# Kernel tuning notes

Hardware: AMD Instinct MI355X
Metric: run time of the kernel (lower is better)

## Reference

```python
import jax, jax.numpy as jnp
import numpy as np

TAU = 0.07
K = 50
EPS = 1e-8


def _flat_norm(x):
    # [B, C, H, W] -> [B*H*W, C], L2-normalized along C
    B, C = x.shape[0], x.shape[1]
    x = jnp.moveaxis(x, 1, -1).reshape(-1, C)
    n = jnp.linalg.norm(x, axis=-1, keepdims=True)
    return x / jnp.maximum(n, 1e-12)


def setup_inputs() -> dict:
    key = jax.random.key(0)
    ks = jax.random.split(key, 5)
    shp = (2, 128, 64, 64)
    lshp = (2, 4, 64, 64)
    return {
        "input": jax.random.normal(ks[0], shp, dtype=jnp.float32),
        "positive": jax.random.normal(ks[1], shp, dtype=jnp.float32),
        "negative": jax.random.normal(ks[2], shp, dtype=jnp.float32),
        "input_logits": jax.random.normal(ks[3], lshp, dtype=jnp.float32),
        "negative_logits": jax.random.normal(ks[4], lshp, dtype=jnp.float32),
    }


def reference(input, positive, negative, input_logits, negative_logits):
    norm_input = _flat_norm(input)        # [N, C]
    norm_positive = _flat_norm(positive)  # [N, C]
    norm_negative = _flat_norm(negative)  # [N, C]

    # check_input: multi-class logits branch (softmax over class dim, then max)
    in_probs = jax.nn.softmax(input_logits, axis=1)
    neg_probs = jax.nn.softmax(negative_logits, axis=1)
    seg_input = jnp.argmax(in_probs, axis=1).reshape(-1)       # [N] int
    seg_negative = jnp.argmax(neg_probs, axis=1).reshape(-1)   # [N] int
    negative_prob = jnp.max(neg_probs, axis=1).reshape(-1)     # [N] float

    # positive cosine similarity (unit vectors -> dot product)
    pos_sim = jnp.sum(norm_input * norm_positive, axis=-1)     # [N]

    # mask[i, j] = (seg_input[j] != seg_negative[i]) * negative_prob[i]
    diff = (seg_input[None, :] != seg_negative[:, None]).astype(jnp.float16)
    masked = diff.astype(jnp.float32) * negative_prob[:, None]  # [N, N]

    # top-k over dim=0 (negatives) for each input column j -> indices [N, K]
    _, idx = jax.lax.top_k(masked.T, K)                         # [N, K]
    sampled = norm_negative[idx]                                # [N, K, C]

    neg_sim = jnp.einsum('nkc,nc->nk', sampled, norm_input)     # [N, K]
    nominator = jnp.exp(pos_sim / TAU)                          # [N]
    denominator = jnp.sum(jnp.exp(neg_sim / TAU), axis=1) + nominator
    loss = -jnp.mean(jnp.log(nominator / (denominator + EPS)))

    alter_sim = jnp.einsum('nkc,nc->nk', sampled, norm_positive)
    alter_den = jnp.sum(jnp.exp(alter_sim / TAU), axis=1) + nominator
    alter_loss = -jnp.mean(jnp.log(nominator / (alter_den + EPS)))

    return loss + alter_loss
```

## Files before the change

### kernel.cpp

```cpp
#include <hip/hip_runtime.h>
#include <math.h>

#define TAU_INV (1.0f / 0.07f)
#define KSEL 50
#define KPAD 64
#define NPIX 8192
#define CCH 128
#define HWSZ 4096
#define NCLS 4
#define EPSL 1e-8f
#define NBINS 1026
#define PXT 32
#define SROW 132

__global__ void __launch_bounds__(256) mega_kernel(
        const float* __restrict__ input, const float* __restrict__ positive,
        const float* __restrict__ negative,
        const float* __restrict__ ilog, const float* __restrict__ nlog,
        float* __restrict__ ni, float* __restrict__ np_, float* __restrict__ nn,
        int* __restrict__ seg_in, int* __restrict__ seg_neg,
        float* __restrict__ neg_prob) {
    __shared__ float tile[CCH][65];
    __shared__ float partial[4][64];
    __shared__ float invn[64];

    int t = threadIdx.x;
    int blk = blockIdx.x;

    if (blk < 384) {
        int tensor = blk >> 7, chunk = blk & 127;
        const float* src = (tensor == 0) ? input : (tensor == 1) ? positive : negative;
        float*       dst = (tensor == 0) ? ni    : (tensor == 1) ? np_      : nn;

        int n0 = chunk * 64;
        int b = n0 >> 12, hw0 = n0 & (HWSZ - 1);
        const float* base = src + (size_t)b * CCH * HWSZ + hw0;

        #pragma unroll
        for (int i = 0; i < 8; ++i) {
            int lin = t + i * 256;
            int c = lin >> 4, hwq = (lin & 15) * 4;
            float4 v = *(const float4*)&base[(size_t)c * HWSZ + hwq];
            tile[c][hwq + 0] = v.x; tile[c][hwq + 1] = v.y;
            tile[c][hwq + 2] = v.z; tile[c][hwq + 3] = v.w;
        }
        __syncthreads();

        int nof = t & 63, part = t >> 6;
        float s = 0.f;
        #pragma unroll
        for (int j = 0; j < 32; ++j) {
            float v = tile[part * 32 + j][nof];
            s += v * v;
        }
        partial[part][nof] = s;
        __syncthreads();
        if (t < 64) {
            float tot = partial[0][t] + partial[1][t] + partial[2][t] + partial[3][t];
            invn[t] = 1.0f / fmaxf(sqrtf(tot), 1e-12f);
        }
        __syncthreads();

        #pragma unroll
        for (int i = 0; i < 8; ++i) {
            int lin = t + i * 256;
            int nf = lin >> 5, cq = (lin & 31) * 4;
            float inv = invn[nf];
            float4 o;
            o.x = tile[cq + 0][nf] * inv;
            o.y = tile[cq + 1][nf] * inv;
            o.z = tile[cq + 2][nf] * inv;
            o.w = tile[cq + 3][nf] * inv;
            *(float4*)&dst[(size_t)(n0 + nf) * CCH + cq] = o;
        }
    } else {
        int n0 = ((blk - 384) * 256 + t) * 4;
        int b = n0 >> 12, hw = n0 & (HWSZ - 1);

        const float* pi = ilog + (size_t)b * NCLS * HWSZ + hw;
        float4 a0 = *(const float4*)&pi[0];
        float4 a1 = *(const float4*)&pi[HWSZ];
        float4 a2 = *(const float4*)&pi[2 * HWSZ];
        float4 a3 = *(const float4*)&pi[3 * HWSZ];
        const float* pn = nlog + (size_t)b * NCLS * HWSZ + hw;
        float4 b0 = *(const float4*)&pn[0];
        float4 b1 = *(const float4*)&pn[HWSZ];
        float4 b2 = *(const float4*)&pn[2 * HWSZ];
        float4 b3 = *(const float4*)&pn[3 * HWSZ];

        int4 si4, sn4; float4 npb;
        const float* A0 = (const float*)&a0; const float* A1 = (const float*)&a1;
        const float* A2 = (const float*)&a2; const float* A3 = (const float*)&a3;
        const float* B0 = (const float*)&b0; const float* B1 = (const float*)&b1;
        const float* B2 = (const float*)&b2; const float* B3 = (const float*)&b3;
        int* SI = (int*)&si4; int* SN = (int*)&sn4; float* NP = (float*)&npb;
        #pragma unroll
        for (int j = 0; j < 4; ++j) {
            float l0 = A0[j], l1 = A1[j], l2 = A2[j], l3 = A3[j];
            int bi = 0; float bv = l0;
            if (l1 > bv) { bv = l1; bi = 1; }
            if (l2 > bv) { bv = l2; bi = 2; }
            if (l3 > bv) { bv = l3; bi = 3; }
            SI[j] = bi;
            float m0 = B0[j], m1 = B1[j], m2 = B2[j], m3 = B3[j];
            int ci = 0; float cv = m0;
            if (m1 > cv) { cv = m1; ci = 1; }
            if (m2 > cv) { cv = m2; ci = 2; }
            if (m3 > cv) { cv = m3; ci = 3; }
            SN[j] = ci;
            float s = expf(m0 - cv) + expf(m1 - cv) + expf(m2 - cv) + expf(m3 - cv);
            NP[j] = 1.0f / s;
        }
        *(int4*)&seg_in[n0] = si4;
        *(int4*)&seg_neg[n0] = sn4;
        *(float4*)&neg_prob[n0] = npb;
    }
}

__global__ void __launch_bounds__(1024) topk_kernel(
        const int* __restrict__ seg_in, const int* __restrict__ seg_neg,
        const float* __restrict__ neg_prob,
        int* __restrict__ topk, int* __restrict__ perm, int* __restrict__ cnt,
        float* __restrict__ out) {
    __shared__ unsigned hist[NBINS];
    __shared__ unsigned coarse[33];
    __shared__ unsigned long long cand[2048];
    __shared__ unsigned above_cnt, cand_cnt, bucket_cnt;
    __shared__ int sB, sc0;

    int c = blockIdx.x, t = threadIdx.x;
    if (c == 0 && t == 0) out[0] = 0.0f;

    for (int i = t; i < NBINS; i += 1024) hist[i] = 0;
    if (t < 33) coarse[t] = 0;
    if (t == 0) { above_cnt = 0; cand_cnt = 0; bucket_cnt = 0; }
    __syncthreads();

    unsigned keys[8]; int bins[8];
    #pragma unroll
    for (int s = 0; s < 2; ++s) {
        int i4 = (t + s * 1024) * 4;
        int4 sn = *(const int4*)&seg_neg[i4];
        int4 sg = *(const int4*)&seg_in[i4];
        float4 npv = *(const float4*)&neg_prob[i4];
        const int* SN = (const int*)&sn;
        const int* SG = (const int*)&sg;
        const float* NP = (const float*)&npv;
        #pragma unroll
        for (int j = 0; j < 4; ++j) {
            float v = (SN[j] != c) ? NP[j] : 0.0f;
            unsigned key = __float_as_uint(v);
            int bin = (key < 0x3E800000u) ? 0 : (int)(1u + ((key - 0x3E800000u) >> 14));
            keys[s * 4 + j] = key; bins[s * 4 + j] = bin;
            atomicAdd(&hist[bin], 1u);
            if (SG[j] == c) {
                unsigned p = atomicAdd(&bucket_cnt, 1u);
                perm[c * NPIX + p] = i4 + j;
            }
        }
    }
    __syncthreads();
    if (t == 0) cnt[c] = (int)bucket_cnt;

    for (int i = t; i < NBINS; i += 1024) atomicAdd(&coarse[i >> 5], hist[i]);
    __syncthreads();

    if (t == 0) {
        unsigned cum = 0; int j = 32;
        for (; j > 0; --j) {
            unsigned h = coarse[j];
            if (cum + h >= KSEL) break;
            cum += h;
        }
        int hi = j * 32 + 31; if (hi > NBINS - 1) hi = NBINS - 1;
        int B = 0;
        for (int b = hi; b >= j * 32; --b) {
            unsigned h = hist[b];
            if (cum + h >= KSEL) { B = b; break; }
            cum += h;
        }
        sB = B; sc0 = (int)cum;
    }
    __syncthreads();
    int B = sB, c0 = sc0;

    #pragma unroll
    for (int s = 0; s < 8; ++s) {
        int i = (t + (s >> 2) * 1024) * 4 + (s & 3);
        if (bins[s] > B) {
            unsigned pos = atomicAdd(&above_cnt, 1u);
            topk[c * KSEL + pos] = i;
        } else if (bins[s] == B) {
            unsigned j = atomicAdd(&cand_cnt, 1u);
            if (j < 2048)
                cand[j] = ((unsigned long long)keys[s] << 32) |
                          (unsigned long long)(0xFFFFFFFFu - (unsigned)i);
        }
    }
    __syncthreads();

    int m = KSEL - c0;
    int cb = (int)cand_cnt; if (cb > 2048) cb = 2048;
    if (t < 64) {
        for (int r = 0; r < m; ++r) {
            unsigned long long best = 0;
            for (int j = t; j < cb; j += 64) {
                unsigned long long v = cand[j];
                if (v > best) best = v;
            }
            #pragma unroll
            for (int off = 32; off; off >>= 1) {
                unsigned long long o = __shfl_xor(best, off);
                if (o > best) best = o;
            }
            if (t == 0) topk[c * KSEL + c0 + r] = (int)(0xFFFFFFFFu - (unsigned)(best & 0xFFFFFFFFull));
            for (int j = t; j < cb; j += 64)
                if (cand[j] == best) cand[j] = 0;
        }
    }
}

__global__ void __launch_bounds__(256) loss_kernel(
        const float* __restrict__ ni, const float* __restrict__ npos,
        const float* __restrict__ nn, const int* __restrict__ topk,
        const int* __restrict__ perm, const int* __restrict__ cnt,
        float* __restrict__ out) {
    __shared__ float Sl[KPAD * SROW];
    __shared__ float Xl[PXT * SROW];
    __shared__ float Pl[PXT * SROW];
    __shared__ float bsum[4];

    int c = blockIdx.y;
    int count = cnt[c];
    int start = blockIdx.x * PXT;
    if (start >= count) return;
    int t = threadIdx.x;

    {
        int row = t >> 2;
        int ch0 = (t & 3) * 32;
        float* dst = &Sl[row * SROW + ch0];
        if (row < KSEL) {
            const float* src = nn + (size_t)topk[c * KSEL + row] * CCH + ch0;
            #pragma unroll
            for (int i = 0; i < 8; ++i)
                ((float4*)dst)[i] = ((const float4*)src)[i];
        } else {
            float4 z = make_float4(0.f, 0.f, 0.f, 0.f);
            #pragma unroll
            for (int i = 0; i < 8; ++i)
                ((float4*)dst)[i] = z;
        }
    }
    {
        int row = t >> 3;
        int slot = start + row;
        int px = perm[c * NPIX + ((slot < count) ? slot : start)];
        int ch0 = (t & 7) * 16;
        const float* sx = ni + (size_t)px * CCH + ch0;
        const float* sp = npos + (size_t)px * CCH + ch0;
        float* dx = &Xl[row * SROW + ch0];
        float* dp = &Pl[row * SROW + ch0];
        #pragma unroll
        for (int i = 0; i < 4; ++i) {
            ((float4*)dx)[i] = ((const float4*)sx)[i];
            ((float4*)dp)[i] = ((const float4*)sp)[i];
        }
    }
    __syncthreads();

    int ktid = t & 7, pxid = t >> 3;
    float acc_i[8] = {0.f, 0.f, 0.f, 0.f, 0.f, 0.f, 0.f, 0.f};
    float acc_p[8] = {0.f, 0.f, 0.f, 0.f, 0.f, 0.f, 0.f, 0.f};
    float ps = 0.f;
    const float* Xr = &Xl[pxid * SROW];
    const float* Pr = &Pl[pxid * SROW];

    #pragma unroll 2
    for (int ch = 0; ch < CCH; ch += 4) {
        float4 xv = *(const float4*)&Xr[ch];
        float4 pv = *(const float4*)&Pr[ch];
        ps += xv.x * pv.x + xv.y * pv.y + xv.z * pv.z + xv.w * pv.w;
        #pragma unroll
        for (int r = 0; r < 8; ++r) {
            float4 sv = *(const float4*)&Sl[(ktid + r * 8) * SROW + ch];
            acc_i[r] += sv.x * xv.x + sv.y * xv.y + sv.z * xv.z + sv.w * xv.w;
            acc_p[r] += sv.x * pv.x + sv.y * pv.y + sv.z * pv.z + sv.w * pv.w;
        }
    }

    float si = 0.f, spp = 0.f;
    #pragma unroll
    for (int r = 0; r < 8; ++r) {
        si  += expf(acc_i[r] * TAU_INV);
        spp += expf(acc_p[r] * TAU_INV);
    }
    #pragma unroll
    for (int off = 1; off < 8; off <<= 1) {
        si  += __shfl_xor(si, off);
        spp += __shfl_xor(spp, off);
    }

    float v = 0.f;
    if (ktid == 0 && (start + pxid) < count) {
        si  -= (float)(KPAD - KSEL);
        spp -= (float)(KPAD - KSEL);
        float nom = expf(ps * TAU_INV);
        float li = -logf(nom / (si + nom + EPSL));
        float lp = -logf(nom / (spp + nom + EPSL));
        v = (li + lp) * (1.0f / (float)NPIX);
    }
    v += __shfl_xor(v, 8);
    v += __shfl_xor(v, 16);
    v += __shfl_xor(v, 32);
    int w = t >> 6;
    if ((t & 63) == 0) bsum[w] = v;
    __syncthreads();
    if (t == 0) atomicAdd(out, bsum[0] + bsum[1] + bsum[2] + bsum[3]);
}

extern "C" void kernel_launch(void* const* d_in, const int* in_sizes, int n_in,
                              void* d_out, int out_size, void* d_ws, size_t ws_size,
                              hipStream_t stream) {
    const float* input      = (const float*)d_in[0];
    const float* positive   = (const float*)d_in[1];
    const float* negative   = (const float*)d_in[2];
    const float* in_logits  = (const float*)d_in[3];
    const float* neg_logits = (const float*)d_in[4];
    float* out = (float*)d_out;

    float* ws  = (float*)d_ws;
    float* ni  = ws;
    float* np_ = ws + 1048576;
    float* nn  = ws + 2097152;
    int*   seg_in   = (int*)(ws + 3145728);
    int*   seg_neg  = seg_in + NPIX;
    float* neg_prob = (float*)(seg_neg + NPIX);
    int*   topk     = (int*)(neg_prob + NPIX);
    int*   cnt      = topk + 256;
    int*   perm     = cnt + 64;

    mega_kernel<<<392, 256, 0, stream>>>(input, positive, negative,
                                         in_logits, neg_logits,
                                         ni, np_, nn, seg_in, seg_neg, neg_prob);
    topk_kernel<<<NCLS, 1024, 0, stream>>>(seg_in, seg_neg, neg_prob,
                                           topk, perm, cnt, out);
    dim3 lgrid(NPIX / PXT, NCLS);
    loss_kernel<<<lgrid, 256, 0, stream>>>(ni, np_, nn, topk, perm, cnt, out);
}
```

Baseline: 98.35 us.

## Fuse segmentation and top-k selection into the normalization kernel

Merges the topk kernel into the prep kernel. Four extra blocks of 256 threads each recompute the argmax and softmax max-prob straight from the logits and run the histogram top-k selection, while the other blocks normalize the features in parallel. This removes one kernel launch and the seg/prob intermediate buffers in global memory. In exchange, each top-k block does the per-pixel work with 256 instead of 1024 threads, and the logits are recomputed redundantly once per class.

```diff
diff --git a/kernel.cpp b/kernel.cpp
--- a/kernel.cpp
+++ b/kernel.cpp
@@ -13,21 +13,35 @@
 #define PXT 32
 #define SROW 132
 
-__global__ void __launch_bounds__(256) mega_kernel(
+__global__ void __launch_bounds__(256) prep_kernel(
         const float* __restrict__ input, const float* __restrict__ positive,
         const float* __restrict__ negative,
         const float* __restrict__ ilog, const float* __restrict__ nlog,
         float* __restrict__ ni, float* __restrict__ np_, float* __restrict__ nn,
-        int* __restrict__ seg_in, int* __restrict__ seg_neg,
-        float* __restrict__ neg_prob) {
-    __shared__ float tile[CCH][65];
-    __shared__ float partial[4][64];
-    __shared__ float invn[64];
+        int* __restrict__ topk, int* __restrict__ perm, int* __restrict__ cnt,
+        float* __restrict__ out) {
+    __shared__ union {
+        struct {
+            float tile[CCH][65];
+            float partial[4][64];
+            float invn[64];
+        } a;
+        struct {
+            unsigned hist[NBINS];
+            unsigned coarse[33];
+            unsigned long long cand[2048];
+            unsigned above_cnt, cand_cnt, bucket_cnt;
+            int sB, sc0;
+        } b;
+    } sm;
 
     int t = threadIdx.x;
-    int blk = blockIdx.x;
-
-    if (blk < 384) {
+    int bid = blockIdx.x;
+
+    if (bid == 0 && t == 0) out[0] = 0.0f;
+
+    if (bid >= NCLS) {
+        int blk = bid - NCLS;
         int tensor = blk >> 7, chunk = blk & 127;
         const float* src = (tensor == 0) ? input : (tensor == 1) ? positive : negative;
         float*       dst = (tensor == 0) ? ni    : (tensor == 1) ? np_      : nn;
@@ -39,10 +53,10 @@
         #pragma unroll
         for (int i = 0; i < 8; ++i) {
             int lin = t + i * 256;
-            int c = lin >> 4, hwq = (lin & 15) * 4;
-            float4 v = *(const float4*)&base[(size_t)c * HWSZ + hwq];
-            tile[c][hwq + 0] = v.x; tile[c][hwq + 1] = v.y;
-            tile[c][hwq + 2] = v.z; tile[c][hwq + 3] = v.w;
+            int cc = lin >> 4, hwq = (lin & 15) * 4;
+            float4 v = *(const float4*)&base[(size_t)cc * HWSZ + hwq];
+            sm.a.tile[cc][hwq + 0] = v.x; sm.a.tile[cc][hwq + 1] = v.y;
+            sm.a.tile[cc][hwq + 2] = v.z; sm.a.tile[cc][hwq + 3] = v.w;
         }
         __syncthreads();
 
@@ -50,14 +64,15 @@
         float s = 0.f;
         #pragma unroll
         for (int j = 0; j < 32; ++j) {
-            float v = tile[part * 32 + j][nof];
+            float v = sm.a.tile[part * 32 + j][nof];
             s += v * v;
         }
-        partial[part][nof] = s;
+        sm.a.partial[part][nof] = s;
         __syncthreads();
         if (t < 64) {
-            float tot = partial[0][t] + partial[1][t] + partial[2][t] + partial[3][t];
-            invn[t] = 1.0f / fmaxf(sqrtf(tot), 1e-12f);
+            float tot = sm.a.partial[0][t] + sm.a.partial[1][t] +
+                        sm.a.partial[2][t] + sm.a.partial[3][t];
+            sm.a.invn[t] = 1.0f / fmaxf(sqrtf(tot), 1e-12f);
         }
         __syncthreads();
 
@@ -65,17 +80,29 @@
         for (int i = 0; i < 8; ++i) {
             int lin = t + i * 256;
             int nf = lin >> 5, cq = (lin & 31) * 4;
-            float inv = invn[nf];
+            float inv = sm.a.invn[nf];
             float4 o;
-            o.x = tile[cq + 0][nf] * inv;
-            o.y = tile[cq + 1][nf] * inv;
-            o.z = tile[cq + 2][nf] * inv;
-            o.w = tile[cq + 3][nf] * inv;
+            o.x = sm.a.tile[cq + 0][nf] * inv;
+            o.y = sm.a.tile[cq + 1][nf] * inv;
+            o.z = sm.a.tile[cq + 2][nf] * inv;
+            o.w = sm.a.tile[cq + 3][nf] * inv;
             *(float4*)&dst[(size_t)(n0 + nf) * CCH + cq] = o;
         }
-    } else {
-        int n0 = ((blk - 384) * 256 + t) * 4;
-        int b = n0 >> 12, hw = n0 & (HWSZ - 1);
+        return;
+    }
+
+    int c = bid;
+
+    for (int i = t; i < NBINS; i += 256) sm.b.hist[i] = 0;
+    if (t < 33) sm.b.coarse[t] = 0;
+    if (t == 0) { sm.b.above_cnt = 0; sm.b.cand_cnt = 0; sm.b.bucket_cnt = 0; }
+    __syncthreads();
+
+    unsigned keys[32];
+    #pragma unroll
+    for (int s = 0; s < 8; ++s) {
+        int i4 = (t + s * 256) * 4;
+        int b = i4 >> 12, hw = i4 & (HWSZ - 1);
 
         const float* pi = ilog + (size_t)b * NCLS * HWSZ + hw;
         float4 a0 = *(const float4*)&pi[0];
@@ -88,12 +115,10 @@
         float4 b2 = *(const float4*)&pn[2 * HWSZ];
         float4 b3 = *(const float4*)&pn[3 * HWSZ];
 
-        int4 si4, sn4; float4 npb;
         const float* A0 = (const float*)&a0; const float* A1 = (const float*)&a1;
         const float* A2 = (const float*)&a2; const float* A3 = (const float*)&a3;
         const float* B0 = (const float*)&b0; const float* B1 = (const float*)&b1;
         const float* B2 = (const float*)&b2; const float* B3 = (const float*)&b3;
-        int* SI = (int*)&si4; int* SN = (int*)&sn4; float* NP = (float*)&npb;
         #pragma unroll
         for (int j = 0; j < 4; ++j) {
             float l0 = A0[j], l1 = A1[j], l2 = A2[j], l3 = A3[j];
@@ -101,111 +126,77 @@
             if (l1 > bv) { bv = l1; bi = 1; }
             if (l2 > bv) { bv = l2; bi = 2; }
             if (l3 > bv) { bv = l3; bi = 3; }
-            SI[j] = bi;
             float m0 = B0[j], m1 = B1[j], m2 = B2[j], m3 = B3[j];
             int ci = 0; float cv = m0;
             if (m1 > cv) { cv = m1; ci = 1; }
             if (m2 > cv) { cv = m2; ci = 2; }
             if (m3 > cv) { cv = m3; ci = 3; }
-            SN[j] = ci;
-            float s = expf(m0 - cv) + expf(m1 - cv) + expf(m2 - cv) + expf(m3 - cv);
-            NP[j] = 1.0f / s;
-        }
-        *(int4*)&seg_in[n0] = si4;
-        *(int4*)&seg_neg[n0] = sn4;
-        *(float4*)&neg_prob[n0] = npb;
-    }
-}
-
-__global__ void __launch_bounds__(1024) topk_kernel(
-        const int* __restrict__ seg_in, const int* __restrict__ seg_neg,
-        const float* __restrict__ neg_prob,
-        int* __restrict__ topk, int* __restrict__ perm, int* __restrict__ cnt,
-        float* __restrict__ out) {
-    __shared__ unsigned hist[NBINS];
-    __shared__ unsigned coarse[33];
-    __shared__ unsigned long long cand[2048];
-    __shared__ unsigned above_cnt, cand_cnt, bucket_cnt;
-    __shared__ int sB, sc0;
-
-    int c = blockIdx.x, t = threadIdx.x;
-    if (c == 0 && t == 0) out[0] = 0.0f;
-
-    for (int i = t; i < NBINS; i += 1024) hist[i] = 0;
-    if (t < 33) coarse[t] = 0;
-    if (t == 0) { above_cnt = 0; cand_cnt = 0; bucket_cnt = 0; }
-    __syncthreads();
-
-    unsigned keys[8]; int bins[8];
-    #pragma unroll
-    for (int s = 0; s < 2; ++s) {
-        int i4 = (t + s * 1024) * 4;
-        int4 sn = *(const int4*)&seg_neg[i4];
-        int4 sg = *(const int4*)&seg_in[i4];
-        float4 npv = *(const float4*)&neg_prob[i4];
-        const int* SN = (const int*)&sn;
-        const int* SG = (const int*)&sg;
-        const float* NP = (const float*)&npv;
-        #pragma unroll
-        for (int j = 0; j < 4; ++j) {
-            float v = (SN[j] != c) ? NP[j] : 0.0f;
+            float ssum = expf(m0 - cv) + expf(m1 - cv) + expf(m2 - cv) + expf(m3 - cv);
+            float npv = 1.0f / ssum;
+
+            float v = (ci != c) ? npv : 0.0f;
             unsigned key = __float_as_uint(v);
+            keys[s * 4 + j] = key;
             int bin = (key < 0x3E800000u) ? 0 : (int)(1u + ((key - 0x3E800000u) >> 14));
-            keys[s * 4 + j] = key; bins[s * 4 + j] = bin;
-            atomicAdd(&hist[bin], 1u);
-            if (SG[j] == c) {
-                unsigned p = atomicAdd(&bucket_cnt, 1u);
+            atomicAdd(&sm.b.hist[bin], 1u);
+            if (bi == c) {
+                unsigned p = atomicAdd(&sm.b.bucket_cnt, 1u);
                 perm[c * NPIX + p] = i4 + j;
             }
         }
     }
     __syncthreads();
-    if (t == 0) cnt[c] = (int)bucket_cnt;
-
-    for (int i = t; i < NBINS; i += 1024) atomicAdd(&coarse[i >> 5], hist[i]);
+    if (t == 0) cnt[c] = (int)sm.b.bucket_cnt;
+
+    for (int i = t; i < NBINS; i += 256) atomicAdd(&sm.b.coarse[i >> 5], sm.b.hist[i]);
     __syncthreads();
 
     if (t == 0) {
         unsigned cum = 0; int j = 32;
         for (; j > 0; --j) {
-            unsigned h = coarse[j];
+            unsigned h = sm.b.coarse[j];
             if (cum + h >= KSEL) break;
             cum += h;
         }
         int hi = j * 32 + 31; if (hi > NBINS - 1) hi = NBINS - 1;
         int B = 0;
         for (int b = hi; b >= j * 32; --b) {
-            unsigned h = hist[b];
+            unsigned h = sm.b.hist[b];
             if (cum + h >= KSEL) { B = b; break; }
             cum += h;
         }
-        sB = B; sc0 = (int)cum;
-    }
-    __syncthreads();
-    int B = sB, c0 = sc0;
+        sm.b.sB = B; sm.b.sc0 = (int)cum;
+    }
+    __syncthreads();
+    int B = sm.b.sB, c0 = sm.b.sc0;
 
     #pragma unroll
     for (int s = 0; s < 8; ++s) {
-        int i = (t + (s >> 2) * 1024) * 4 + (s & 3);
-        if (bins[s] > B) {
-            unsigned pos = atomicAdd(&above_cnt, 1u);
-            topk[c * KSEL + pos] = i;
-        } else if (bins[s] == B) {
-            unsigned j = atomicAdd(&cand_cnt, 1u);
-            if (j < 2048)
-                cand[j] = ((unsigned long long)keys[s] << 32) |
-                          (unsigned long long)(0xFFFFFFFFu - (unsigned)i);
+        #pragma unroll
+        for (int j = 0; j < 4; ++j) {
+            unsigned key = keys[s * 4 + j];
+            int bin = (key < 0x3E800000u) ? 0 : (int)(1u + ((key - 0x3E800000u) >> 14));
+            int i = (t + s * 256) * 4 + j;
+            if (bin > B) {
+                unsigned pos = atomicAdd(&sm.b.above_cnt, 1u);
+                topk[c * KSEL + pos] = i;
+            } else if (bin == B) {
+                unsigned jj = atomicAdd(&sm.b.cand_cnt, 1u);
+                if (jj < 2048)
+                    sm.b.cand[jj] = ((unsigned long long)key << 32) |
+                                    (unsigned long long)(0xFFFFFFFFu - (unsigned)i);
+            }
         }
     }
     __syncthreads();
 
     int m = KSEL - c0;
-    int cb = (int)cand_cnt; if (cb > 2048) cb = 2048;
+    int cb = (int)sm.b.cand_cnt; if (cb > 2048) cb = 2048;
     if (t < 64) {
         for (int r = 0; r < m; ++r) {
             unsigned long long best = 0;
             for (int j = t; j < cb; j += 64) {
-                unsigned long long v = cand[j];
+                unsigned long long v = sm.b.cand[j];
                 if (v > best) best = v;
             }
             #pragma unroll
@@ -213,9 +204,10 @@
                 unsigned long long o = __shfl_xor(best, off);
                 if (o > best) best = o;
             }
-            if (t == 0) topk[c * KSEL + c0 + r] = (int)(0xFFFFFFFFu - (unsigned)(best & 0xFFFFFFFFull));
+            if (t == 0) topk[c * KSEL + c0 + r] =
+                (int)(0xFFFFFFFFu - (unsigned)(best & 0xFFFFFFFFull));
             for (int j = t; j < cb; j += 64)
-                if (cand[j] == best) cand[j] = 0;
+                if (sm.b.cand[j] == best) sm.b.cand[j] = 0;
         }
     }
 }
@@ -333,18 +325,13 @@
     float* ni  = ws;
     float* np_ = ws + 1048576;
     float* nn  = ws + 2097152;
-    int*   seg_in   = (int*)(ws + 3145728);
-    int*   seg_neg  = seg_in + NPIX;
-    float* neg_prob = (float*)(seg_neg + NPIX);
-    int*   topk     = (int*)(neg_prob + NPIX);
-    int*   cnt      = topk + 256;
-    int*   perm     = cnt + 64;
-
-    mega_kernel<<<392, 256, 0, stream>>>(input, positive, negative,
-                                         in_logits, neg_logits,
-                                         ni, np_, nn, seg_in, seg_neg, neg_prob);
-    topk_kernel<<<NCLS, 1024, 0, stream>>>(seg_in, seg_neg, neg_prob,
-                                           topk, perm, cnt, out);
+    int*   topk = (int*)(ws + 3145728);
+    int*   cnt  = topk + 256;
+    int*   perm = cnt + 64;
+
+    prep_kernel<<<384 + NCLS, 256, 0, stream>>>(input, positive, negative,
+                                                in_logits, neg_logits,
+                                                ni, np_, nn, topk, perm, cnt, out);
     dim3 lgrid(NPIX / PXT, NCLS);
     loss_kernel<<<lgrid, 256, 0, stream>>>(ni, np_, nn, topk, perm, cnt, out);
 }
```

Result: slower. 106.8 us (+8.6%).
